# Performance work log

Hardware: AMD Instinct MI355X
Metric: run time of the kernel (lower is better)

Reference implementation:

```python
import jax, jax.numpy as jnp
import numpy as np
from jax import lax

B, OBS, E, H = 65536, 20, 64, 64


def setup_inputs() -> dict:
    key = jax.random.key(0)
    ks = jax.random.split(key, 13)
    s = 0.1
    inp = {
        "obs_traj": jax.random.normal(ks[0], (B, OBS, 2), jnp.float32),
        "W_emb": jax.random.normal(ks[1], (E, 2), jnp.float32) * s,
        "b_emb": jax.random.normal(ks[2], (E,), jnp.float32) * s,
        "Wih_e": jax.random.normal(ks[3], (4 * H, E), jnp.float32) * s,
        "Whh_e": jax.random.normal(ks[4], (4 * H, H), jnp.float32) * s,
        "bih_e": jax.random.normal(ks[5], (4 * H,), jnp.float32) * s,
        "bhh_e": jax.random.normal(ks[6], (4 * H,), jnp.float32) * s,
        "Wih_d": jax.random.normal(ks[7], (4 * H, E), jnp.float32) * s,
        "Whh_d": jax.random.normal(ks[8], (4 * H, H), jnp.float32) * s,
        "bih_d": jax.random.normal(ks[9], (4 * H,), jnp.float32) * s,
        "bhh_d": jax.random.normal(ks[10], (4 * H,), jnp.float32) * s,
        "W_fc": jax.random.normal(ks[11], (2, H), jnp.float32) * s,
        "b_fc": jax.random.normal(ks[12], (2,), jnp.float32) * s,
        "pred_len": 12,
    }
    return inp


def _lstm_step(x, h, c, Wih, Whh, b):
    # PyTorch LSTM gate order: i, f, g, o
    g = x @ Wih.T + h @ Whh.T + b  # [B, 4H]
    i, f, gg, o = jnp.split(g, 4, axis=-1)
    c2 = jax.nn.sigmoid(f) * c + jax.nn.sigmoid(i) * jnp.tanh(gg)
    h2 = jax.nn.sigmoid(o) * jnp.tanh(c2)
    return h2, c2


def reference(obs_traj, W_emb, b_emb, Wih_e, Whh_e, bih_e, bhh_e,
              Wih_d, Whh_d, bih_d, bhh_d, W_fc, b_fc, pred_len):
    bsz = obs_traj.shape[0]
    dt = obs_traj.dtype
    # Encoder: embed all observed steps at once, then scan the LSTM over time.
    emb = jax.nn.relu(obs_traj @ W_emb.T + b_emb)  # [B, OBS, E]
    b_e = bih_e + bhh_e
    h0 = jnp.zeros((bsz, H), dt)
    c0 = jnp.zeros((bsz, H), dt)

    def enc_step(carry, x_t):
        h, c = carry
        h, c = _lstm_step(x_t, h, c, Wih_e, Whh_e, b_e)
        return (h, c), None

    (h, c), _ = lax.scan(enc_step, (h0, c0), jnp.swapaxes(emb, 0, 1))

    b_d = bih_d + bhh_d
    dec_in = jax.nn.relu(obs_traj[:, -1, :] @ W_emb.T + b_emb)  # [B, E]

    def dec_step(carry, _):
        h, c, x = carry
        h, c = _lstm_step(x, h, c, Wih_d, Whh_d, b_d)
        pred = h @ W_fc.T + b_fc  # [B, 2]
        nxt = jax.nn.relu(pred @ W_emb.T + b_emb)
        return (h, c, nxt), pred

    _, preds = lax.scan(dec_step, (h, c, dec_in), None, length=pred_len)
    return jnp.swapaxes(preds, 0, 1)  # [B, pred_len, 2]
```

## Files before the change

kernel.cpp:

```cpp
#include <hip/hip_runtime.h>

typedef __bf16 bf16x8 __attribute__((ext_vector_type(8)));
typedef float  f32x4  __attribute__((ext_vector_type(4)));

constexpr int BATCH = 65536;
constexpr int OBS   = 20;
constexpr int PRED  = 12;
constexpr int BT    = 128;
constexpr int AST   = 136;

static_assert(BATCH % BT == 0, "grid must tile batch exactly");

template <int N> struct ic { static constexpr int v = N; };

__device__ __forceinline__ float fast_sigmoid(float x) {
    float e = __builtin_amdgcn_exp2f(-1.4426950408889634f * x);
    return __builtin_amdgcn_rcpf(1.0f + e);
}
__device__ __forceinline__ float fast_tanh(float x) {
    float e = __builtin_amdgcn_exp2f(2.8853900817779268f * x);
    return 1.0f - 2.0f * __builtin_amdgcn_rcpf(1.0f + e);
}

struct SmallW {
    float bcomb_e[256];
    float bcomb_d[256];
    float wemb[128];
    float bemb[64];
    float wfc[128];
    float bfc[2];
};

__global__ __launch_bounds__(256, 2)
void vanilla_lstm(const float* __restrict__ obs,
                  const float* __restrict__ W_emb, const float* __restrict__ b_emb,
                  const float* __restrict__ Wih_e, const float* __restrict__ Whh_e,
                  const float* __restrict__ bih_e, const float* __restrict__ bhh_e,
                  const float* __restrict__ Wih_d, const float* __restrict__ Whh_d,
                  const float* __restrict__ bih_d, const float* __restrict__ bhh_d,
                  const float* __restrict__ W_fc,  const float* __restrict__ b_fc,
                  float* __restrict__ out)
{
    __shared__ __align__(16) __bf16 As[BT * AST];
    __shared__ __align__(16) float  obs_s[BT * OBS * 2];
    __shared__ SmallW sw;

    const int tid  = threadIdx.x;
    const int wv   = tid >> 6;
    const int lane = tid & 63;
    const int m    = lane & 15;
    const int q    = lane >> 4;
    const int wblk = wv * 16;
    const size_t gRow0 = (size_t)blockIdx.x * BT;

    {
        const float4* src = (const float4*)(obs + gRow0 * (OBS * 2));
        float4* dst = (float4*)obs_s;
        #pragma unroll
        for (int i = 0; i < (BT * OBS * 2 / 4) / 256; ++i)
            dst[tid + i * 256] = src[tid + i * 256];
    }
    {
        sw.bcomb_e[tid] = bih_e[tid] + bhh_e[tid];
        sw.bcomb_d[tid] = bih_d[tid] + bhh_d[tid];
        if (tid < 128) { sw.wemb[tid] = W_emb[tid]; sw.wfc[tid] = W_fc[tid]; }
        if (tid < 64)  sw.bemb[tid] = b_emb[tid];
        if (tid < 2)   sw.bfc[tid]  = b_fc[tid];
    }
    {
        uint4 z; z.x = z.y = z.z = z.w = 0u;
        uint4* p = (uint4*)As;
        constexpr int NV = BT * AST * 2 / 16;
        #pragma unroll
        for (int i = 0; i < (NV + 255) / 256; ++i) {
            int idx = tid + i * 256;
            if (idx < NV) p[idx] = z;
        }
    }

    bf16x8 bfr[4][4];
    auto load_bfr = [&](const float* Wih, const float* Whh) {
        #pragma unroll
        for (int c = 0; c < 4; ++c) {
            const int n = (wv + 4 * c) * 16 + m;
            #pragma unroll
            for (int kt = 0; kt < 4; ++kt) {
                const float* s = (kt < 2) ? (Wih + n * 64 + kt * 32 + q * 8)
                                          : (Whh + n * 64 + (kt - 2) * 32 + q * 8);
                bf16x8 v;
                #pragma unroll
                for (int j = 0; j < 8; ++j) v[j] = (__bf16)s[j];
                bfr[c][kt] = v;
            }
        }
    };
    load_bfr(Wih_e, Whh_e);

    f32x4 cst[8];
    #pragma unroll
    for (int i = 0; i < 8; ++i) cst[i] = f32x4{0.f, 0.f, 0.f, 0.f};

    __syncthreads();

    float bias[4];
    #pragma unroll
    for (int c = 0; c < 4; ++c) bias[c] = sw.bcomb_e[(wv + 4 * c) * 16 + m];

    auto write_emb_enc = [&](int row, int t) {
        const float o0 = obs_s[row * (OBS * 2) + t * 2 + 0];
        const float o1 = obs_s[row * (OBS * 2) + t * 2 + 1];
        #pragma unroll
        for (int h8 = 0; h8 < 2; ++h8) {
            bf16x8 v;
            #pragma unroll
            for (int j = 0; j < 8; ++j) {
                const int e = wblk + h8 * 8 + j;
                float x = o0 * sw.wemb[2 * e] + o1 * sw.wemb[2 * e + 1] + sw.bemb[e];
                v[j] = (__bf16)fmaxf(x, 0.f);
            }
            *(bf16x8*)&As[row * AST + wblk + h8 * 8] = v;
        }
    };

    write_emb_enc(lane, 0);
    write_emb_enc(64 + lane, 0);
    __syncthreads();

    auto do_chunk = [&](auto C) {
        constexpr int chunk = decltype(C)::v;
        const int cb = chunk * 64;
        f32x4 acc[4][4];
        #pragma unroll
        for (int rt = 0; rt < 4; ++rt) {
            #pragma unroll
            for (int c = 0; c < 4; ++c)
                acc[rt][c] = f32x4{bias[c], bias[c], bias[c], bias[c]};
        }
        #pragma unroll
        for (int kt = 0; kt < 4; ++kt) {
            bf16x8 af[4];
            #pragma unroll
            for (int rt = 0; rt < 4; ++rt)
                af[rt] = *(const bf16x8*)&As[(cb + rt * 16 + m) * AST + kt * 32 + q * 8];
            #pragma unroll
            for (int rt = 0; rt < 4; ++rt) {
                #pragma unroll
                for (int c = 0; c < 4; ++c)
                    acc[rt][c] = __builtin_amdgcn_mfma_f32_16x16x32_bf16(
                        af[rt], bfr[c][kt], acc[rt][c], 0, 0, 0);
            }
        }
        __syncthreads();
        #pragma unroll
        for (int rt = 0; rt < 4; ++rt) {
            #pragma unroll
            for (int r = 0; r < 4; ++r) {
                const float gi = acc[rt][0][r];
                const float gf = acc[rt][1][r];
                const float gg = acc[rt][2][r];
                const float go = acc[rt][3][r];
                const float cPrev = cst[chunk * 4 + rt][r];
                const float cNew  = fast_sigmoid(gf) * cPrev + fast_sigmoid(gi) * fast_tanh(gg);
                const float hNew  = fast_sigmoid(go) * fast_tanh(cNew);
                cst[chunk * 4 + rt][r] = cNew;
                As[(cb + rt * 16 + q * 4 + r) * AST + 64 + wblk + m] = (__bf16)hNew;
            }
        }
    };

    for (int t = 0; t < OBS; ++t) {
        do_chunk(ic<0>{});
        if (t + 1 < OBS) write_emb_enc(lane, t + 1);
        do_chunk(ic<1>{});
        if (t + 1 < OBS) write_emb_enc(64 + lane, t + 1);
    }

    load_bfr(Wih_d, Whh_d);
    #pragma unroll
    for (int c = 0; c < 4; ++c) bias[c] = sw.bcomb_d[(wv + 4 * c) * 16 + m];

    for (int td = 0; td < PRED; ++td) {
        do_chunk(ic<0>{});
        do_chunk(ic<1>{});
        __syncthreads();
        if (tid < BT) {
            const int row = tid;
            float p0 = sw.bfc[0], p1 = sw.bfc[1];
            #pragma unroll
            for (int e8 = 0; e8 < 8; ++e8) {
                bf16x8 hv = *(const bf16x8*)&As[row * AST + 64 + e8 * 8];
                #pragma unroll
                for (int j = 0; j < 8; ++j) {
                    const float h = (float)hv[j];
                    p0 += h * sw.wfc[e8 * 8 + j];
                    p1 += h * sw.wfc[64 + e8 * 8 + j];
                }
            }
            const size_t ob = ((gRow0 + row) * PRED + td) * 2;
            out[ob + 0] = p0;
            out[ob + 1] = p1;
            if (td + 1 < PRED) {
                #pragma unroll
                for (int e8 = 0; e8 < 8; ++e8) {
                    bf16x8 v;
                    #pragma unroll
                    for (int j = 0; j < 8; ++j) {
                        const int e = e8 * 8 + j;
                        float x = p0 * sw.wemb[2 * e] + p1 * sw.wemb[2 * e + 1] + sw.bemb[e];
                        v[j] = (__bf16)fmaxf(x, 0.f);
                    }
                    *(bf16x8*)&As[row * AST + e8 * 8] = v;
                }
            }
        }
        __syncthreads();
    }
}

extern "C" void kernel_launch(void* const* d_in, const int* in_sizes, int n_in,
                              void* d_out, int out_size, void* d_ws, size_t ws_size,
                              hipStream_t stream) {
    (void)in_sizes; (void)n_in; (void)d_ws; (void)ws_size; (void)out_size;
    const float* obs   = (const float*)d_in[0];
    const float* W_emb = (const float*)d_in[1];
    const float* b_emb = (const float*)d_in[2];
    const float* Wih_e = (const float*)d_in[3];
    const float* Whh_e = (const float*)d_in[4];
    const float* bih_e = (const float*)d_in[5];
    const float* bhh_e = (const float*)d_in[6];
    const float* Wih_d = (const float*)d_in[7];
    const float* Whh_d = (const float*)d_in[8];
    const float* bih_d = (const float*)d_in[9];
    const float* bhh_d = (const float*)d_in[10];
    const float* W_fc  = (const float*)d_in[11];
    const float* b_fc  = (const float*)d_in[12];
    float* o = (float*)d_out;

    dim3 grid(BATCH / BT), block(256);
    hipLaunchKernelGGL(vanilla_lstm, grid, block, 0, stream,
                       obs, W_emb, b_emb, Wih_e, Whh_e, bih_e, bhh_e,
                       Wih_d, Whh_d, bih_d, bhh_d, W_fc, b_fc, o);
}
```

Baseline: 336.3 us.

## Software-pipeline LSTM chunks, transpose MFMA operands, and parallelize decoder prediction

Restructures the per-step schedule so the gate GEMM of one 64-row chunk overlaps the activation update of the other chunk, trimming barriers per step. MFMA operands are swapped so each lane writes four contiguous h values as a bf16x4 store instead of scattered scalar stores. The decoder FC projection now uses all 256 threads with a shuffle reduction, and embedding is split per chunk. Observations are read directly from global memory instead of being staged in LDS, which cuts LDS use (possibly raising occupancy) but puts global loads inside the recurrence.

```diff
diff --git a/kernel.cpp b/kernel.cpp
--- a/kernel.cpp
+++ b/kernel.cpp
@@ -1,7 +1,9 @@
 #include <hip/hip_runtime.h>
 
 typedef __bf16 bf16x8 __attribute__((ext_vector_type(8)));
+typedef __bf16 bf16x4 __attribute__((ext_vector_type(4)));
 typedef float  f32x4  __attribute__((ext_vector_type(4)));
+typedef float  f32x2  __attribute__((ext_vector_type(2)));
 
 constexpr int BATCH = 65536;
 constexpr int OBS   = 20;
@@ -9,26 +11,19 @@
 constexpr int BT    = 128;
 constexpr int AST   = 136;
 
-static_assert(BATCH % BT == 0, "grid must tile batch exactly");
-
-template <int N> struct ic { static constexpr int v = N; };
-
-__device__ __forceinline__ float fast_sigmoid(float x) {
-    float e = __builtin_amdgcn_exp2f(-1.4426950408889634f * x);
-    return __builtin_amdgcn_rcpf(1.0f + e);
-}
-__device__ __forceinline__ float fast_tanh(float x) {
-    float e = __builtin_amdgcn_exp2f(2.8853900817779268f * x);
-    return 1.0f - 2.0f * __builtin_amdgcn_rcpf(1.0f + e);
+__device__ __forceinline__ float sigm(float x) {
+    return __builtin_amdgcn_rcpf(1.0f + __builtin_amdgcn_exp2f(x * -1.4426950408889634f));
+}
+__device__ __forceinline__ float tanh_(float x) {
+    return 1.0f - 2.0f * __builtin_amdgcn_rcpf(1.0f + __builtin_amdgcn_exp2f(x * 2.8853900817779268f));
 }
 
 struct SmallW {
-    float bcomb_e[256];
-    float bcomb_d[256];
-    float wemb[128];
-    float bemb[64];
-    float wfc[128];
-    float bfc[2];
+    float  bcomb_e[256];
+    float  bcomb_d[256];
+    float4 embc[64];
+    float  wfc[128];
+    float  bfc[2];
 };
 
 __global__ __launch_bounds__(256, 2)
@@ -42,7 +37,7 @@
                   float* __restrict__ out)
 {
     __shared__ __align__(16) __bf16 As[BT * AST];
-    __shared__ __align__(16) float  obs_s[BT * OBS * 2];
+    __shared__ __align__(16) float  pred_s[BT * 2];
     __shared__ SmallW sw;
 
     const int tid  = threadIdx.x;
@@ -53,43 +48,35 @@
     const int wblk = wv * 16;
     const size_t gRow0 = (size_t)blockIdx.x * BT;
 
-    {
-        const float4* src = (const float4*)(obs + gRow0 * (OBS * 2));
-        float4* dst = (float4*)obs_s;
-        #pragma unroll
-        for (int i = 0; i < (BT * OBS * 2 / 4) / 256; ++i)
-            dst[tid + i * 256] = src[tid + i * 256];
-    }
-    {
-        sw.bcomb_e[tid] = bih_e[tid] + bhh_e[tid];
-        sw.bcomb_d[tid] = bih_d[tid] + bhh_d[tid];
-        if (tid < 128) { sw.wemb[tid] = W_emb[tid]; sw.wfc[tid] = W_fc[tid]; }
-        if (tid < 64)  sw.bemb[tid] = b_emb[tid];
-        if (tid < 2)   sw.bfc[tid]  = b_fc[tid];
-    }
+    sw.bcomb_e[tid] = bih_e[tid] + bhh_e[tid];
+    sw.bcomb_d[tid] = bih_d[tid] + bhh_d[tid];
+    if (tid < 64)  sw.embc[tid] = make_float4(W_emb[2 * tid], W_emb[2 * tid + 1], b_emb[tid], 0.f);
+    if (tid < 128) sw.wfc[tid]  = W_fc[tid];
+    if (tid < 2)   sw.bfc[tid]  = b_fc[tid];
+
     {
         uint4 z; z.x = z.y = z.z = z.w = 0u;
         uint4* p = (uint4*)As;
         constexpr int NV = BT * AST * 2 / 16;
         #pragma unroll
-        for (int i = 0; i < (NV + 255) / 256; ++i) {
-            int idx = tid + i * 256;
-            if (idx < NV) p[idx] = z;
-        }
+        for (int i = 0; i < NV / 256; ++i) p[tid + i * 256] = z;
+        if (tid < (NV % 256)) p[tid + (NV / 256) * 256] = z;
     }
 
     bf16x8 bfr[4][4];
     auto load_bfr = [&](const float* Wih, const float* Whh) {
         #pragma unroll
         for (int c = 0; c < 4; ++c) {
-            const int n = (wv + 4 * c) * 16 + m;
+            const int n = c * 64 + wblk + m;
             #pragma unroll
             for (int kt = 0; kt < 4; ++kt) {
                 const float* s = (kt < 2) ? (Wih + n * 64 + kt * 32 + q * 8)
                                           : (Whh + n * 64 + (kt - 2) * 32 + q * 8);
+                float4 a = *(const float4*)s;
+                float4 b = *(const float4*)(s + 4);
                 bf16x8 v;
-                #pragma unroll
-                for (int j = 0; j < 8; ++j) v[j] = (__bf16)s[j];
+                v[0] = (__bf16)a.x; v[1] = (__bf16)a.y; v[2] = (__bf16)a.z; v[3] = (__bf16)a.w;
+                v[4] = (__bf16)b.x; v[5] = (__bf16)b.y; v[6] = (__bf16)b.z; v[7] = (__bf16)b.w;
                 bfr[c][kt] = v;
             }
         }
@@ -102,118 +89,142 @@
 
     __syncthreads();
 
-    float bias[4];
-    #pragma unroll
-    for (int c = 0; c < 4; ++c) bias[c] = sw.bcomb_e[(wv + 4 * c) * 16 + m];
-
-    auto write_emb_enc = [&](int row, int t) {
-        const float o0 = obs_s[row * (OBS * 2) + t * 2 + 0];
-        const float o1 = obs_s[row * (OBS * 2) + t * 2 + 1];
+    f32x4 bias4[4];
+    auto load_bias = [&](const float* bc) {
+        #pragma unroll
+        for (int c = 0; c < 4; ++c)
+            bias4[c] = *(const f32x4*)&bc[c * 64 + wblk + q * 4];
+    };
+    load_bias(sw.bcomb_e);
+
+    f32x4 acc[4][4];
+
+    auto gemm = [&](int chunk) {
+        #pragma unroll
+        for (int nt = 0; nt < 4; ++nt)
+            #pragma unroll
+            for (int c = 0; c < 4; ++c)
+                acc[nt][c] = bias4[c];
+        #pragma unroll
+        for (int kt = 0; kt < 4; ++kt) {
+            bf16x8 af[4];
+            #pragma unroll
+            for (int nt = 0; nt < 4; ++nt)
+                af[nt] = *(const bf16x8*)&As[(chunk * 64 + nt * 16 + m) * AST + kt * 32 + q * 8];
+            #pragma unroll
+            for (int nt = 0; nt < 4; ++nt)
+                #pragma unroll
+                for (int c = 0; c < 4; ++c)
+                    acc[nt][c] = __builtin_amdgcn_mfma_f32_16x16x32_bf16(
+                        bfr[c][kt], af[nt], acc[nt][c], 0, 0, 0);
+        }
+    };
+
+    auto update = [&](int chunk) {
+        #pragma unroll
+        for (int nt = 0; nt < 4; ++nt) {
+            const int row = chunk * 64 + nt * 16 + m;
+            f32x4 ci = cst[chunk * 4 + nt];
+            bf16x4 h4;
+            #pragma unroll
+            for (int r = 0; r < 4; ++r) {
+                const float cN = sigm(acc[nt][1][r]) * ci[r]
+                               + sigm(acc[nt][0][r]) * tanh_(acc[nt][2][r]);
+                ci[r] = cN;
+                h4[r] = (__bf16)(sigm(acc[nt][3][r]) * tanh_(cN));
+            }
+            cst[chunk * 4 + nt] = ci;
+            *(bf16x4*)&As[row * AST + 64 + wblk + q * 4] = h4;
+        }
+    };
+
+    auto emb_row = [&](int row, float o0, float o1) {
         #pragma unroll
         for (int h8 = 0; h8 < 2; ++h8) {
             bf16x8 v;
             #pragma unroll
             for (int j = 0; j < 8; ++j) {
-                const int e = wblk + h8 * 8 + j;
-                float x = o0 * sw.wemb[2 * e] + o1 * sw.wemb[2 * e + 1] + sw.bemb[e];
-                v[j] = (__bf16)fmaxf(x, 0.f);
+                float4 wc = sw.embc[wblk + h8 * 8 + j];
+                v[j] = (__bf16)fmaxf(fmaf(o0, wc.x, fmaf(o1, wc.y, wc.z)), 0.f);
             }
             *(bf16x8*)&As[row * AST + wblk + h8 * 8] = v;
         }
     };
 
-    write_emb_enc(lane, 0);
-    write_emb_enc(64 + lane, 0);
+    const float* obr0 = obs + (gRow0 + lane) * (OBS * 2);
+    const float* obr1 = obs + (gRow0 + 64 + lane) * (OBS * 2);
+
+    {
+        f32x2 o0 = *(const f32x2*)obr0;
+        f32x2 o1 = *(const f32x2*)obr1;
+        emb_row(lane, o0[0], o0[1]);
+        emb_row(64 + lane, o1[0], o1[1]);
+    }
     __syncthreads();
-
-    auto do_chunk = [&](auto C) {
-        constexpr int chunk = decltype(C)::v;
-        const int cb = chunk * 64;
-        f32x4 acc[4][4];
-        #pragma unroll
-        for (int rt = 0; rt < 4; ++rt) {
-            #pragma unroll
-            for (int c = 0; c < 4; ++c)
-                acc[rt][c] = f32x4{bias[c], bias[c], bias[c], bias[c]};
-        }
-        #pragma unroll
-        for (int kt = 0; kt < 4; ++kt) {
-            bf16x8 af[4];
-            #pragma unroll
-            for (int rt = 0; rt < 4; ++rt)
-                af[rt] = *(const bf16x8*)&As[(cb + rt * 16 + m) * AST + kt * 32 + q * 8];
-            #pragma unroll
-            for (int rt = 0; rt < 4; ++rt) {
-                #pragma unroll
-                for (int c = 0; c < 4; ++c)
-                    acc[rt][c] = __builtin_amdgcn_mfma_f32_16x16x32_bf16(
-                        af[rt], bfr[c][kt], acc[rt][c], 0, 0, 0);
-            }
-        }
-        __syncthreads();
-        #pragma unroll
-        for (int rt = 0; rt < 4; ++rt) {
-            #pragma unroll
-            for (int r = 0; r < 4; ++r) {
-                const float gi = acc[rt][0][r];
-                const float gf = acc[rt][1][r];
-                const float gg = acc[rt][2][r];
-                const float go = acc[rt][3][r];
-                const float cPrev = cst[chunk * 4 + rt][r];
-                const float cNew  = fast_sigmoid(gf) * cPrev + fast_sigmoid(gi) * fast_tanh(gg);
-                const float hNew  = fast_sigmoid(go) * fast_tanh(cNew);
-                cst[chunk * 4 + rt][r] = cNew;
-                As[(cb + rt * 16 + q * 4 + r) * AST + 64 + wblk + m] = (__bf16)hNew;
-            }
-        }
-    };
+    gemm(0);
 
     for (int t = 0; t < OBS; ++t) {
-        do_chunk(ic<0>{});
-        if (t + 1 < OBS) write_emb_enc(lane, t + 1);
-        do_chunk(ic<1>{});
-        if (t + 1 < OBS) write_emb_enc(64 + lane, t + 1);
+        __syncthreads();
+        f32x2 on0{0.f, 0.f};
+        if (t + 1 < OBS) on0 = *(const f32x2*)(obr0 + (t + 1) * 2);
+        update(0);
+        gemm(1);
+        if (t + 1 < OBS) emb_row(lane, on0[0], on0[1]);
+        __syncthreads();
+        f32x2 on1{0.f, 0.f};
+        if (t + 1 < OBS) on1 = *(const f32x2*)(obr1 + (t + 1) * 2);
+        update(1);
+        if (t + 1 < OBS) {
+            gemm(0);
+            emb_row(64 + lane, on1[0], on1[1]);
+        }
     }
 
     load_bfr(Wih_d, Whh_d);
-    #pragma unroll
-    for (int c = 0; c < 4; ++c) bias[c] = sw.bcomb_d[(wv + 4 * c) * 16 + m];
+    load_bias(sw.bcomb_d);
+    gemm(0);
+
+    auto pred_phase = [&](int chunk, int td) {
+        const int prow = chunk * 64 + (tid >> 2);
+        const int comp = (tid >> 1) & 1, half = tid & 1;
+        const int cb = half * 32;
+        float p = 0.f;
+        #pragma unroll
+        for (int e8 = 0; e8 < 4; ++e8) {
+            bf16x8 hv = *(const bf16x8*)&As[prow * AST + 64 + cb + e8 * 8];
+            f32x4 w0 = *(const f32x4*)&sw.wfc[comp * 64 + cb + e8 * 8];
+            f32x4 w1 = *(const f32x4*)&sw.wfc[comp * 64 + cb + e8 * 8 + 4];
+            p += (float)hv[0] * w0[0] + (float)hv[1] * w0[1] + (float)hv[2] * w0[2] + (float)hv[3] * w0[3]
+               + (float)hv[4] * w1[0] + (float)hv[5] * w1[1] + (float)hv[6] * w1[2] + (float)hv[7] * w1[3];
+        }
+        p += __shfl_xor(p, 1, 64);
+        if (half == 0) {
+            p += sw.bfc[comp];
+            pred_s[prow * 2 + comp] = p;
+            out[((gRow0 + prow) * PRED + td) * 2 + comp] = p;
+        }
+    };
+    auto emb_dec = [&](int chunk) {
+        const int row = chunk * 64 + lane;
+        f32x2 pv = *(const f32x2*)&pred_s[row * 2];
+        emb_row(row, pv[0], pv[1]);
+    };
 
     for (int td = 0; td < PRED; ++td) {
-        do_chunk(ic<0>{});
-        do_chunk(ic<1>{});
-        __syncthreads();
-        if (tid < BT) {
-            const int row = tid;
-            float p0 = sw.bfc[0], p1 = sw.bfc[1];
-            #pragma unroll
-            for (int e8 = 0; e8 < 8; ++e8) {
-                bf16x8 hv = *(const bf16x8*)&As[row * AST + 64 + e8 * 8];
-                #pragma unroll
-                for (int j = 0; j < 8; ++j) {
-                    const float h = (float)hv[j];
-                    p0 += h * sw.wfc[e8 * 8 + j];
-                    p1 += h * sw.wfc[64 + e8 * 8 + j];
-                }
-            }
-            const size_t ob = ((gRow0 + row) * PRED + td) * 2;
-            out[ob + 0] = p0;
-            out[ob + 1] = p1;
-            if (td + 1 < PRED) {
-                #pragma unroll
-                for (int e8 = 0; e8 < 8; ++e8) {
-                    bf16x8 v;
-                    #pragma unroll
-                    for (int j = 0; j < 8; ++j) {
-                        const int e = e8 * 8 + j;
-                        float x = p0 * sw.wemb[2 * e] + p1 * sw.wemb[2 * e + 1] + sw.bemb[e];
-                        v[j] = (__bf16)fmaxf(x, 0.f);
-                    }
-                    *(bf16x8*)&As[row * AST + e8 * 8] = v;
-                }
-            }
-        }
-        __syncthreads();
+        __syncthreads();
+        update(0);
+        gemm(1);
+        __syncthreads();
+        update(1);
+        pred_phase(0, td);
+        __syncthreads();
+        pred_phase(1, td);
+        if (td + 1 < PRED) emb_dec(0);
+        __syncthreads();
+        if (td + 1 < PRED) {
+            emb_dec(1);
+            gemm(0);
+        }
     }
 }
 
```

Measured after the change: 307.4 us. 1.09x faster.
